# Kernel tuning notes

Measured on AMD Instinct MI355X. Metric: run time of the kernel, lower is better.

## Reference

```python
import jax, jax.numpy as jnp
from jax import lax
import numpy as np

B, C, H, W = 4, 256, 100, 100
K = 9  # num_points; deform kernel is [1, K], padding [0, K//2]


def conv2d(x, w, b, pad):
    # x: [B,Cin,H,W], w: [Cout,Cin,kh,kw]
    y = lax.conv_general_dilated(x, w, (1, 1), [(pad, pad), (pad, pad)],
                                 dimension_numbers=('NCHW', 'OIHW', 'NCHW'))
    return y + b[None, :, None, None]


def bilinear_sample(img, ys, xs):
    # img: [B,C,H,W]; ys, xs: [B,H,W] float sample coords; zero padding outside.
    Bs, Cs, Hs, Ws = img.shape
    y0f = jnp.floor(ys)
    x0f = jnp.floor(xs)
    wy = (ys - y0f)[:, None]  # [B,1,H,W]
    wx = (xs - x0f)[:, None]
    y0 = y0f.astype(jnp.int32)
    x0 = x0f.astype(jnp.int32)
    img_flat = img.reshape(Bs, Cs, Hs * Ws)

    def gather(yi, xi):
        valid = ((yi >= 0) & (yi < Hs) & (xi >= 0) & (xi < Ws))
        yc = jnp.clip(yi, 0, Hs - 1)
        xc = jnp.clip(xi, 0, Ws - 1)
        idx = (yc * Ws + xc).reshape(Bs, 1, Hs * Ws)
        v = jnp.take_along_axis(img_flat, idx, axis=2).reshape(Bs, Cs, Hs, Ws)
        return v * valid[:, None].astype(img.dtype)

    v00 = gather(y0, x0)
    v01 = gather(y0, x0 + 1)
    v10 = gather(y0 + 1, x0)
    v11 = gather(y0 + 1, x0 + 1)
    return (v00 * (1 - wy) * (1 - wx) + v01 * (1 - wy) * wx
            + v10 * wy * (1 - wx) + v11 * wy * wx)


def deform_conv_1xK(x, w, offset):
    # x: [B,C,H,W], w: [Cout,Cin,1,K], offset: [B,2K,H,W] with (dy,dx) per point.
    Bs, Cs, Hs, Ws = x.shape
    off = offset.reshape(Bs, K, 2, Hs, Ws)
    hh = jnp.arange(Hs, dtype=x.dtype)[:, None]
    ww = jnp.arange(Ws, dtype=x.dtype)[None, :]
    out = jnp.zeros((Bs, w.shape[0], Hs, Ws), dtype=x.dtype)
    for k in range(K):  # small fixed kernel loop
        ys = hh + off[:, k, 0]                    # kh=0, pad_h=0
        xs = ww + (k - K // 2) + off[:, k, 1]     # kw=k, pad_w=K//2
        s = bilinear_sample(x, ys, xs)            # [B,C,H,W]
        out = out + jnp.einsum('bchw,oc->bohw', s, w[:, :, 0, k])
    return out


def base_offset():
    dx = np.arange(-(K // 2), K // 2 + 1, dtype=np.float32)
    dy = np.zeros_like(dx)
    base = np.stack([dy, dx], axis=1).reshape(-1)  # [y0,x0,y1,x1,...]
    return jnp.asarray(base).reshape(1, 2 * K, 1, 1)


def setup_inputs() -> dict:
    key = jax.random.key(0)
    ks = jax.random.split(key, 8)
    return {
        'cls_feat': jax.random.normal(ks[0], (B, C, H, W), jnp.float32),
        'reg_feat': jax.random.normal(ks[1], (B, C, H, W), jnp.float32),
        'scale': jnp.float32(1.0),
        'offset_conv_w': 0.01 * jax.random.normal(ks[2], (C, C, 3, 3), jnp.float32),
        'offset_conv_b': jnp.zeros((C,), jnp.float32),
        'offset_out_w': 0.01 * jax.random.normal(ks[3], (2 * K, C, 1, 1), jnp.float32),
        'offset_out_b': jnp.zeros((2 * K,), jnp.float32),
        'cls_dcn_w': 0.02 * jax.random.normal(ks[4], (C, C, 1, K), jnp.float32),
        'reg_dcn_w': 0.02 * jax.random.normal(ks[5], (C, C, 1, K), jnp.float32),
    }


def reference(cls_feat, reg_feat, scale, offset_conv_w, offset_conv_b,
              offset_out_w, offset_out_b, cls_dcn_w, reg_dcn_w):
    # offset branch: ConvModule(3x3, ReLU) -> 1x1 conv -> learnable scalar
    t = jax.nn.relu(conv2d(reg_feat, offset_conv_w, offset_conv_b, 1))
    pts = scale * conv2d(t, offset_out_w, offset_out_b, 0)   # [B,2K,H,W]
    off = pts - base_offset()
    cls_out = jax.nn.relu(deform_conv_1xK(cls_feat, cls_dcn_w, off))
    reg_out = jax.nn.relu(deform_conv_1xK(reg_feat, reg_dcn_w, off))
    return (cls_out, reg_out, pts)
```

## Files before the change

### kernel.cpp

```cpp
#include <hip/hip_runtime.h>
#include <cstddef>

#define Bn 4
#define Cn 256
#define Hn 100
#define Wn 100
#define HWn 10000
#define Kn 9

typedef __attribute__((ext_vector_type(8))) short short8v;
typedef __attribute__((ext_vector_type(4))) float floatx4;
typedef __attribute__((ext_vector_type(4))) unsigned short ushort4v;

__device__ __forceinline__ float b2f(short s) {
  return __uint_as_float(((unsigned)(unsigned short)s) << 16);
}
__device__ __forceinline__ unsigned short f2bf(float f) {
  unsigned u = __float_as_uint(f);
  unsigned r = (u + 0x7FFF + ((u >> 16) & 1)) >> 16;
  return (unsigned short)r;
}
__device__ __forceinline__ void gload_lds16(const ushort* g, ushort* l) {
  __builtin_amdgcn_global_load_lds(
      (const __attribute__((address_space(1))) unsigned int*)(g),
      (__attribute__((address_space(3))) unsigned int*)(l), 16, 0, 0);
}

__global__ __launch_bounds__(256) void wtAll_kernel(
    const float* __restrict__ wcls, const float* __restrict__ wreg,
    const float* __restrict__ wconv, ushort* __restrict__ wtAll)
{
  int bk = blockIdx.x;
  int cc = bk & 7;
  int kk = (bk >> 3) % 9;
  int br = bk / 72;
  const float* w = (br == 0) ? wcls : (br == 1) ? wreg : wconv;
  ushort* dst = wtAll + (size_t)bk * 8192;
  for (int idx = threadIdx.x; idx < 8192; idx += 256) {
    int ot = idx >> 9;
    int l  = (idx >> 3) & 63;
    int j  = idx & 7;
    int o  = ot * 16 + (l & 15);
    int c  = cc * 32 + ((l >> 4) << 3) + j;
    dst[idx] = f2bf(w[((size_t)o * Cn + c) * Kn + kk]);
  }
}

__global__ __launch_bounds__(256) void ftrans_kernel(
    const float* __restrict__ clsf, const float* __restrict__ regf,
    ushort* __restrict__ ft)
{
  const int p0 = blockIdx.x * 32;
  const int c0 = blockIdx.y * 32;
  const int z  = blockIdx.z;
  const int br = z >> 2, b = z & 3;
  const float* src = (br ? regf : clsf) + (size_t)b * Cn * HWn;
  __shared__ float tl[32][33];
  const int tid = threadIdx.x;
  for (int i = tid; i < 1024; i += 256) {
    int c = i >> 5, p = i & 31;
    int pp = p0 + p;
    tl[p][c] = (pp < HWn) ? src[(size_t)(c0 + c) * HWn + pp] : 0.f;
  }
  __syncthreads();
  int p = tid >> 3;
  int c = (tid & 7) * 4;
  int pp = p0 + p;
  if (pp < HWn) {
    ushort4v v;
    v.x = f2bf(tl[p][c + 0]);
    v.y = f2bf(tl[p][c + 1]);
    v.z = f2bf(tl[p][c + 2]);
    v.w = f2bf(tl[p][c + 3]);
    *(ushort4v*)(ft + ((size_t)z * HWn + pp) * Cn + c0 + c) = v;
  }
}

__global__ __launch_bounds__(256) void conv3x3_offset_kernel(
    const ushort* __restrict__ ft, const ushort* __restrict__ wtC,
    const float* __restrict__ ocb, const float* __restrict__ oow,
    const float* __restrict__ oob, const float* __restrict__ scale_p,
    float* __restrict__ pts)
{
  const int p0  = blockIdx.x * 64;
  const int b   = blockIdx.z;
  const int tid = threadIdx.x;
  const int wv  = tid >> 6;
  const int lane = tid & 63;

  __shared__ ushort al[8192];
  __shared__ ushort sl[2048];
  __shared__ ushort tl[Cn * 64];

  floatx4 acc[4][4]{};

  const ushort* ftb = ft + (size_t)(4 + b) * HWn * Cn;

  const int px = p0 + lane;
  const bool pvalid = px < HWn;
  const int pxc = pvalid ? px : 0;
  const int y  = pxc / Wn;
  const int x  = pxc - y * Wn;
  const int sidx = (((lane >> 4) * 64) + (lane & 15) + (wv << 4)) * 8;

  for (int tap = 0; tap < 9; ++tap) {
    const int dy = tap / 3 - 1, dx = tap % 3 - 1;
    const int yy = y + dy, xx = x + dx;
    const bool valid = pvalid && (unsigned)yy < (unsigned)Hn
                              && (unsigned)xx < (unsigned)Wn;
    const int pofs = valid ? (yy * Wn + xx) * Cn : 0;

    for (int cc = 0; cc < 8; ++cc) {
      __syncthreads();
      {
        const ushort* src = wtC + (((size_t)tap * 8 + cc) << 13) + tid * 8;
#pragma unroll
        for (int i = 0; i < 4; ++i)
          gload_lds16(src + i * 2048, al + tid * 8 + i * 2048);
      }
      {
        short8v v{};
        if (valid) v = *(const short8v*)(ftb + pofs + cc * 32 + (wv << 3));
        *(short8v*)(sl + sidx) = v;
      }
      __syncthreads();
      short8v fb[4];
#pragma unroll
      for (int nt = 0; nt < 4; ++nt)
        fb[nt] = *(const short8v*)(sl + (nt * 64 + lane) * 8);
#pragma unroll
      for (int mt = 0; mt < 4; ++mt) {
        short8v fa = *(const short8v*)(al + (((wv * 4 + mt) * 64) + lane) * 8);
#pragma unroll
        for (int nt = 0; nt < 4; ++nt)
          acc[mt][nt] = __builtin_amdgcn_mfma_f32_16x16x32_bf16(
              fa, fb[nt], acc[mt][nt], 0, 0, 0);
      }
    }
  }

#pragma unroll
  for (int mt = 0; mt < 4; ++mt) {
    int o = wv * 64 + mt * 16 + ((lane >> 4) << 2);
#pragma unroll
    for (int nt = 0; nt < 4; ++nt) {
      int pcol = nt * 16 + (lane & 15);
      floatx4 a4 = acc[mt][nt];
#pragma unroll
      for (int r = 0; r < 4; ++r) {
        float v = a4[r] + ocb[o + r];
        v = v > 0.f ? v : 0.f;
        tl[(o + r) * 64 + pcol] = f2bf(v);
      }
    }
  }
  __syncthreads();

  const int jw = __builtin_amdgcn_readfirstlane(tid >> 6);
  const int pp = tid & 63;
  const float s = *scale_p;
  if (p0 + pp < HWn) {
    for (int j = jw; j < 18; j += 4) {
      float a = oob[j];
      const float* wrow = oow + (size_t)j * Cn;
      for (int c = 0; c < Cn; ++c)
        a += wrow[c] * b2f(tl[c * 64 + pp]);
      pts[((size_t)b * 18 + j) * HWn + p0 + pp] = s * a;
    }
  }
}

__global__ __launch_bounds__(256) void deform_mfma_kernel(
    const ushort* __restrict__ ft, const ushort* __restrict__ wtA,
    const float* __restrict__ pts, float* __restrict__ out)
{
  const int p0  = blockIdx.x * 64;
  const int z   = blockIdx.z;
  const int br  = z >> 2, b = z & 3;
  const int tid = threadIdx.x;
  const int wv  = tid >> 6;
  const int lane = tid & 63;

  __shared__ ushort al[8192];
  __shared__ ushort sl[2048];

  floatx4 acc[4][4]{};

  const ushort* ftb = ft + (size_t)z * HWn * Cn;
  const float*  pb  = pts + (size_t)b * 18 * HWn;
  const ushort* wA  = wtA + (size_t)br * 9 * 8 * 8192;

  const int px = p0 + lane;
  const bool pvalid = px < HWn;
  const int pxc = pvalid ? px : 0;
  const int hy  = pxc / Wn;
  const int wx0 = pxc - hy * Wn;
  const int sidx = (((lane >> 4) * 64) + (lane & 15) + (wv << 4)) * 8;

  for (int k = 0; k < Kn; ++k) {
    float w00 = 0, w01 = 0, w10 = 0, w11 = 0;
    int i00 = 0, i01 = 0, i10 = 0, i11 = 0;
    {
      float py  = pb[(size_t)(2 * k) * HWn + pxc];
      float pxo = pb[(size_t)(2 * k + 1) * HWn + pxc];
      float offx = pxo - (float)(k - 4);
      float ys   = (float)hy + py;
      float xsf  = (float)(wx0 + (k - 4)) + offx;
      float y0f = floorf(ys), x0f = floorf(xsf);
      float wy = ys - y0f, wx = xsf - x0f;
      int y0 = (int)y0f, x0 = (int)x0f;
      int y1 = y0 + 1, x1 = x0 + 1;
      bool vy0 = (unsigned)y0 < (unsigned)Hn, vy1 = (unsigned)y1 < (unsigned)Hn;
      bool vx0 = (unsigned)x0 < (unsigned)Wn, vx1 = (unsigned)x1 < (unsigned)Wn;
      int yc0 = min(max(y0, 0), Hn - 1), yc1 = min(max(y1, 0), Hn - 1);
      int xc0 = min(max(x0, 0), Wn - 1), xc1 = min(max(x1, 0), Wn - 1);
      i00 = (yc0 * Wn + xc0) * Cn; i01 = (yc0 * Wn + xc1) * Cn;
      i10 = (yc1 * Wn + xc0) * Cn; i11 = (yc1 * Wn + xc1) * Cn;
      float oy = 1.f - wy, ox = 1.f - wx;
      bool pv = pvalid;
      w00 = (pv && vy0 && vx0) ? oy * ox : 0.f;
      w01 = (pv && vy0 && vx1) ? oy * wx : 0.f;
      w10 = (pv && vy1 && vx0) ? wy * ox : 0.f;
      w11 = (pv && vy1 && vx1) ? wy * wx : 0.f;
    }

    for (int cc = 0; cc < 8; ++cc) {
      __syncthreads();
      {
        const ushort* src = wA + (((size_t)k * 8 + cc) << 13) + tid * 8;
#pragma unroll
        for (int i = 0; i < 4; ++i)
          gload_lds16(src + i * 2048, al + tid * 8 + i * 2048);
      }
      {
        const ushort* fbase = ftb + cc * 32 + (wv << 3);
        short8v c00 = *(const short8v*)(fbase + i00);
        short8v c01 = *(const short8v*)(fbase + i01);
        short8v c10 = *(const short8v*)(fbase + i10);
        short8v c11 = *(const short8v*)(fbase + i11);
        short8v r;
#pragma unroll
        for (int jj = 0; jj < 8; ++jj) {
          float v = w00 * b2f(c00[jj]) + w01 * b2f(c01[jj])
                  + w10 * b2f(c10[jj]) + w11 * b2f(c11[jj]);
          r[jj] = (short)f2bf(v);
        }
        *(short8v*)(sl + sidx) = r;
      }
      __syncthreads();
      short8v fb[4];
#pragma unroll
      for (int nt = 0; nt < 4; ++nt)
        fb[nt] = *(const short8v*)(sl + (nt * 64 + lane) * 8);
#pragma unroll
      for (int mt = 0; mt < 4; ++mt) {
        short8v fa = *(const short8v*)(al + (((wv * 4 + mt) * 64) + lane) * 8);
#pragma unroll
        for (int nt = 0; nt < 4; ++nt)
          acc[mt][nt] = __builtin_amdgcn_mfma_f32_16x16x32_bf16(
              fa, fb[nt], acc[mt][nt], 0, 0, 0);
      }
    }
  }

  float* ob = out + (size_t)br * Bn * Cn * HWn + (size_t)b * Cn * HWn;
#pragma unroll
  for (int mt = 0; mt < 4; ++mt) {
    int o = wv * 64 + mt * 16 + ((lane >> 4) << 2);
#pragma unroll
    for (int nt = 0; nt < 4; ++nt) {
      int p = p0 + nt * 16 + (lane & 15);
      if (p < HWn) {
        floatx4 a4 = acc[mt][nt];
#pragma unroll
        for (int r = 0; r < 4; ++r) {
          float v = a4[r];
          ob[(size_t)(o + r) * HWn + p] = v > 0.f ? v : 0.f;
        }
      }
    }
  }
}

extern "C" void kernel_launch(void* const* d_in, const int* in_sizes, int n_in,
                              void* d_out, int out_size, void* d_ws, size_t ws_size,
                              hipStream_t stream) {
  const float* cls_feat = (const float*)d_in[0];
  const float* reg_feat = (const float*)d_in[1];
  const float* scale    = (const float*)d_in[2];
  const float* ocw      = (const float*)d_in[3];
  const float* ocb      = (const float*)d_in[4];
  const float* oow      = (const float*)d_in[5];
  const float* oob      = (const float*)d_in[6];
  const float* wcls     = (const float*)d_in[7];
  const float* wreg     = (const float*)d_in[8];

  float* out_all = (float*)d_out;
  float* pts     = out_all + (size_t)2 * Bn * Cn * HWn;

  ushort* ft    = (ushort*)d_ws;
  ushort* wtAll = (ushort*)((char*)d_ws + (size_t)8 * HWn * Cn * 2);
  ushort* wtC   = wtAll + (size_t)2 * 9 * 8 * 8192;

  wtAll_kernel<<<dim3(216), 256, 0, stream>>>(wcls, wreg, ocw, wtAll);
  ftrans_kernel<<<dim3(313, 8, 8), 256, 0, stream>>>(cls_feat, reg_feat, ft);
  conv3x3_offset_kernel<<<dim3(157, 1, 4), 256, 0, stream>>>(
      ft, wtC, ocb, oow, oob, scale, pts);
  deform_mfma_kernel<<<dim3(157, 1, 8), 256, 0, stream>>>(
      ft, wtAll, pts, out_all);
}
```

Before: 591.5 us.

## Double-buffer LDS in conv and deform kernels and use MFMA for offset 1x1

Both the 3x3 offset conv and the deformable conv kernels now double-buffer weight and sampled-feature tiles in LDS. Global loads and bilinear gathers for the next chunk are issued before the current chunk's MFMAs, which removes one barrier per iteration and hides load latency. The 1x1 offset projection, previously a scalar loop over 256 channels per output, now runs as a bf16 MFMA with weights pre-packed by an extra block in the weight-prep kernel. This raises LDS use and register pressure, and rounds the 1x1 weights to bf16.

Result: faster. 512.9 us (-13.3%).

```diff
diff --git a/kernel.cpp b/kernel.cpp
--- a/kernel.cpp
+++ b/kernel.cpp
@@ -28,9 +28,22 @@
 
 __global__ __launch_bounds__(256) void wtAll_kernel(
     const float* __restrict__ wcls, const float* __restrict__ wreg,
-    const float* __restrict__ wconv, ushort* __restrict__ wtAll)
+    const float* __restrict__ wconv, const float* __restrict__ oow,
+    ushort* __restrict__ wtAll, ushort* __restrict__ oowA)
 {
   int bk = blockIdx.x;
+  if (bk == 216) {
+    for (int idx = threadIdx.x; idx < 8192; idx += 256) {
+      int j = idx & 7;
+      int l = (idx >> 3) & 63;
+      int q = idx >> 9;
+      int cc = q >> 1, ot = q & 1;
+      int o = ot * 16 + (l & 15);
+      int c = cc * 32 + ((l >> 4) << 3) + j;
+      oowA[idx] = (o < 18) ? f2bf(oow[(size_t)o * Cn + c]) : 0;
+    }
+    return;
+  }
   int cc = bk & 7;
   int kk = (bk >> 3) % 9;
   int br = bk / 72;
@@ -78,7 +91,7 @@
 
 __global__ __launch_bounds__(256) void conv3x3_offset_kernel(
     const ushort* __restrict__ ft, const ushort* __restrict__ wtC,
-    const float* __restrict__ ocb, const float* __restrict__ oow,
+    const float* __restrict__ ocb, const ushort* __restrict__ oowA,
     const float* __restrict__ oob, const float* __restrict__ scale_p,
     float* __restrict__ pts)
 {
@@ -88,9 +101,9 @@
   const int wv  = tid >> 6;
   const int lane = tid & 63;
 
-  __shared__ ushort al[8192];
-  __shared__ ushort sl[2048];
-  __shared__ ushort tl[Cn * 64];
+  __shared__ ushort smem[20480];
+  ushort* al = smem;
+  ushort* sl = smem + 16384;
 
   floatx4 acc[4][4]{};
 
@@ -103,71 +116,95 @@
   const int x  = pxc - y * Wn;
   const int sidx = (((lane >> 4) * 64) + (lane & 15) + (wv << 4)) * 8;
 
-  for (int tap = 0; tap < 9; ++tap) {
-    const int dy = tap / 3 - 1, dx = tap % 3 - 1;
-    const int yy = y + dy, xx = x + dx;
-    const bool valid = pvalid && (unsigned)yy < (unsigned)Hn
-                              && (unsigned)xx < (unsigned)Wn;
-    const int pofs = valid ? (yy * Wn + xx) * Cn : 0;
-
-    for (int cc = 0; cc < 8; ++cc) {
-      __syncthreads();
-      {
-        const ushort* src = wtC + (((size_t)tap * 8 + cc) << 13) + tid * 8;
-#pragma unroll
-        for (int i = 0; i < 4; ++i)
-          gload_lds16(src + i * 2048, al + tid * 8 + i * 2048);
+  int pofs = 0; bool valid = false;
+  auto tapgeo = [&](int tap) {
+    int dy = tap / 3 - 1, dx = tap % 3 - 1;
+    int yy = y + dy, xx = x + dx;
+    valid = pvalid && (unsigned)yy < (unsigned)Hn && (unsigned)xx < (unsigned)Wn;
+    pofs = valid ? (yy * Wn + xx) * Cn : 0;
+  };
+
+  short8v cv{};
+  tapgeo(0);
+  if (valid) cv = *(const short8v*)(ftb + pofs + (wv << 3));
+  {
+    const ushort* srcw = wtC + tid * 8;
+#pragma unroll
+    for (int i = 0; i < 4; ++i)
+      gload_lds16(srcw + i * 2048, al + tid * 8 + i * 2048);
+  }
+  *(short8v*)(sl + sidx) = cv;
+
+  for (int t = 0; t < 72; ++t) {
+    __syncthreads();
+    const int buf = t & 1, nb = buf ^ 1;
+    if (t < 71) {
+      const int t1 = t + 1, cc1 = t1 & 7;
+      if (cc1 == 0) tapgeo(t1 >> 3);
+      cv = short8v{};
+      if (valid) cv = *(const short8v*)(ftb + pofs + cc1 * 32 + (wv << 3));
+      const ushort* srcw = wtC + ((size_t)t1 << 13) + tid * 8;
+#pragma unroll
+      for (int i = 0; i < 4; ++i)
+        gload_lds16(srcw + i * 2048, al + nb * 8192 + tid * 8 + i * 2048);
+    }
+    short8v fbv[4];
+#pragma unroll
+    for (int nt = 0; nt < 4; ++nt)
+      fbv[nt] = *(const short8v*)(sl + buf * 2048 + (nt * 64 + lane) * 8);
+#pragma unroll
+    for (int mt = 0; mt < 4; ++mt) {
+      short8v fa = *(const short8v*)(al + buf * 8192 + (((wv * 4 + mt) * 64) + lane) * 8);
+#pragma unroll
+      for (int nt = 0; nt < 4; ++nt)
+        acc[mt][nt] = __builtin_amdgcn_mfma_f32_16x16x32_bf16(
+            fa, fbv[nt], acc[mt][nt], 0, 0, 0);
+    }
+    if (t < 71) *(short8v*)(sl + nb * 2048 + sidx) = cv;
+  }
+
+  __syncthreads();
+  ushort* tl = smem;
+#pragma unroll
+  for (int mt = 0; mt < 4; ++mt) {
+    int ob = wv * 64 + mt * 16 + ((lane >> 4) << 2);
+    floatx4 bv = *(const floatx4*)(ocb + ob);
+#pragma unroll
+    for (int nt = 0; nt < 4; ++nt) {
+      int pxl = nt * 16 + (lane & 15);
+      floatx4 a4 = acc[mt][nt];
+#pragma unroll
+      for (int rp = 0; rp < 4; rp += 2) {
+        float v0 = a4[rp]     + bv[rp];     v0 = v0 > 0.f ? v0 : 0.f;
+        float v1 = a4[rp + 1] + bv[rp + 1]; v1 = v1 > 0.f ? v1 : 0.f;
+        unsigned pk = (unsigned)f2bf(v0) | ((unsigned)f2bf(v1) << 16);
+        *(unsigned*)(tl + pxl * 264 + ob + rp) = pk;
       }
-      {
-        short8v v{};
-        if (valid) v = *(const short8v*)(ftb + pofs + cc * 32 + (wv << 3));
-        *(short8v*)(sl + sidx) = v;
-      }
-      __syncthreads();
-      short8v fb[4];
-#pragma unroll
-      for (int nt = 0; nt < 4; ++nt)
-        fb[nt] = *(const short8v*)(sl + (nt * 64 + lane) * 8);
-#pragma unroll
-      for (int mt = 0; mt < 4; ++mt) {
-        short8v fa = *(const short8v*)(al + (((wv * 4 + mt) * 64) + lane) * 8);
-#pragma unroll
-        for (int nt = 0; nt < 4; ++nt)
-          acc[mt][nt] = __builtin_amdgcn_mfma_f32_16x16x32_bf16(
-              fa, fb[nt], acc[mt][nt], 0, 0, 0);
-      }
-    }
-  }
-
-#pragma unroll
-  for (int mt = 0; mt < 4; ++mt) {
-    int o = wv * 64 + mt * 16 + ((lane >> 4) << 2);
-#pragma unroll
-    for (int nt = 0; nt < 4; ++nt) {
-      int pcol = nt * 16 + (lane & 15);
-      floatx4 a4 = acc[mt][nt];
-#pragma unroll
-      for (int r = 0; r < 4; ++r) {
-        float v = a4[r] + ocb[o + r];
-        v = v > 0.f ? v : 0.f;
-        tl[(o + r) * 64 + pcol] = f2bf(v);
-      }
     }
   }
   __syncthreads();
 
-  const int jw = __builtin_amdgcn_readfirstlane(tid >> 6);
-  const int pp = tid & 63;
+  floatx4 ap[2]{};
+#pragma unroll
+  for (int cc = 0; cc < 8; ++cc) {
+    short8v fbp = *(const short8v*)(tl + (wv * 16 + (lane & 15)) * 264
+                                    + cc * 32 + ((lane >> 4) << 3));
+#pragma unroll
+    for (int ot = 0; ot < 2; ++ot) {
+      short8v faw = *(const short8v*)(oowA + (((cc * 2 + ot) * 64) + lane) * 8);
+      ap[ot] = __builtin_amdgcn_mfma_f32_16x16x32_bf16(faw, fbp, ap[ot], 0, 0, 0);
+    }
+  }
   const float s = *scale_p;
-  if (p0 + pp < HWn) {
-    for (int j = jw; j < 18; j += 4) {
-      float a = oob[j];
-      const float* wrow = oow + (size_t)j * Cn;
-      for (int c = 0; c < Cn; ++c)
-        a += wrow[c] * b2f(tl[c * 64 + pp]);
-      pts[((size_t)b * 18 + j) * HWn + p0 + pp] = s * a;
-    }
-  }
+  const int pp = p0 + wv * 16 + (lane & 15);
+#pragma unroll
+  for (int ot = 0; ot < 2; ++ot)
+#pragma unroll
+    for (int r = 0; r < 4; ++r) {
+      int j = ot * 16 + ((lane >> 4) << 2) + r;
+      if (j < 18 && pp < HWn)
+        pts[((size_t)b * 18 + j) * HWn + pp] = s * (ap[ot][r] + oob[j]);
+    }
 }
 
 __global__ __launch_bounds__(256) void deform_mfma_kernel(
@@ -181,8 +218,9 @@
   const int wv  = tid >> 6;
   const int lane = tid & 63;
 
-  __shared__ ushort al[8192];
-  __shared__ ushort sl[2048];
+  __shared__ ushort smem[20480];
+  ushort* al = smem;
+  ushort* sl = smem + 16384;
 
   floatx4 acc[4][4]{};
 
@@ -197,69 +235,100 @@
   const int wx0 = pxc - hy * Wn;
   const int sidx = (((lane >> 4) * 64) + (lane & 15) + (wv << 4)) * 8;
 
-  for (int k = 0; k < Kn; ++k) {
-    float w00 = 0, w01 = 0, w10 = 0, w11 = 0;
-    int i00 = 0, i01 = 0, i10 = 0, i11 = 0;
-    {
-      float py  = pb[(size_t)(2 * k) * HWn + pxc];
-      float pxo = pb[(size_t)(2 * k + 1) * HWn + pxc];
-      float offx = pxo - (float)(k - 4);
-      float ys   = (float)hy + py;
-      float xsf  = (float)(wx0 + (k - 4)) + offx;
-      float y0f = floorf(ys), x0f = floorf(xsf);
-      float wy = ys - y0f, wx = xsf - x0f;
-      int y0 = (int)y0f, x0 = (int)x0f;
-      int y1 = y0 + 1, x1 = x0 + 1;
-      bool vy0 = (unsigned)y0 < (unsigned)Hn, vy1 = (unsigned)y1 < (unsigned)Hn;
-      bool vx0 = (unsigned)x0 < (unsigned)Wn, vx1 = (unsigned)x1 < (unsigned)Wn;
-      int yc0 = min(max(y0, 0), Hn - 1), yc1 = min(max(y1, 0), Hn - 1);
-      int xc0 = min(max(x0, 0), Wn - 1), xc1 = min(max(x1, 0), Wn - 1);
-      i00 = (yc0 * Wn + xc0) * Cn; i01 = (yc0 * Wn + xc1) * Cn;
-      i10 = (yc1 * Wn + xc0) * Cn; i11 = (yc1 * Wn + xc1) * Cn;
-      float oy = 1.f - wy, ox = 1.f - wx;
-      bool pv = pvalid;
-      w00 = (pv && vy0 && vx0) ? oy * ox : 0.f;
-      w01 = (pv && vy0 && vx1) ? oy * wx : 0.f;
-      w10 = (pv && vy1 && vx0) ? wy * ox : 0.f;
-      w11 = (pv && vy1 && vx1) ? wy * wx : 0.f;
-    }
-
-    for (int cc = 0; cc < 8; ++cc) {
-      __syncthreads();
-      {
-        const ushort* src = wA + (((size_t)k * 8 + cc) << 13) + tid * 8;
-#pragma unroll
-        for (int i = 0; i < 4; ++i)
-          gload_lds16(src + i * 2048, al + tid * 8 + i * 2048);
+  float w00 = 0, w01 = 0, w10 = 0, w11 = 0;
+  int i00 = 0, i01 = 0, i10 = 0, i11 = 0;
+  auto bilinear = [&](int k, float py, float pxo) {
+    float offx = pxo - (float)(k - 4);
+    float ys   = (float)hy + py;
+    float xsf  = (float)(wx0 + (k - 4)) + offx;
+    float y0f = floorf(ys), x0f = floorf(xsf);
+    float wy = ys - y0f, wx = xsf - x0f;
+    int y0 = (int)y0f, x0 = (int)x0f;
+    int y1 = y0 + 1, x1 = x0 + 1;
+    bool vy0 = (unsigned)y0 < (unsigned)Hn, vy1 = (unsigned)y1 < (unsigned)Hn;
+    bool vx0 = (unsigned)x0 < (unsigned)Wn, vx1 = (unsigned)x1 < (unsigned)Wn;
+    int yc0 = min(max(y0, 0), Hn - 1), yc1 = min(max(y1, 0), Hn - 1);
+    int xc0 = min(max(x0, 0), Wn - 1), xc1 = min(max(x1, 0), Wn - 1);
+    i00 = (yc0 * Wn + xc0) * Cn; i01 = (yc0 * Wn + xc1) * Cn;
+    i10 = (yc1 * Wn + xc0) * Cn; i11 = (yc1 * Wn + xc1) * Cn;
+    float oy = 1.f - wy, ox = 1.f - wx;
+    w00 = (pvalid && vy0 && vx0) ? oy * ox : 0.f;
+    w01 = (pvalid && vy0 && vx1) ? oy * wx : 0.f;
+    w10 = (pvalid && vy1 && vx0) ? wy * ox : 0.f;
+    w11 = (pvalid && vy1 && vx1) ? wy * wx : 0.f;
+  };
+
+  float pyN = pb[pxc];
+  float pxN = pb[(size_t)HWn + pxc];
+
+  bilinear(0, pyN, pxN);
+  pyN = pb[(size_t)2 * HWn + pxc];
+  pxN = pb[(size_t)3 * HWn + pxc];
+  short8v c00, c01, c10, c11;
+  {
+    const ushort* fbase = ftb + (wv << 3);
+    c00 = *(const short8v*)(fbase + i00);
+    c01 = *(const short8v*)(fbase + i01);
+    c10 = *(const short8v*)(fbase + i10);
+    c11 = *(const short8v*)(fbase + i11);
+    const ushort* srcw = wA + tid * 8;
+#pragma unroll
+    for (int i = 0; i < 4; ++i)
+      gload_lds16(srcw + i * 2048, al + tid * 8 + i * 2048);
+    short8v r;
+#pragma unroll
+    for (int jj = 0; jj < 8; ++jj) {
+      float v = w00 * b2f(c00[jj]) + w01 * b2f(c01[jj])
+              + w10 * b2f(c10[jj]) + w11 * b2f(c11[jj]);
+      r[jj] = (short)f2bf(v);
+    }
+    *(short8v*)(sl + sidx) = r;
+  }
+
+  for (int t = 0; t < 72; ++t) {
+    __syncthreads();
+    const int buf = t & 1, nb = buf ^ 1;
+    const bool more = t < 71;
+    if (more) {
+      const int t1 = t + 1, k1 = t1 >> 3, cc1 = t1 & 7;
+      if (cc1 == 0) {
+        bilinear(k1, pyN, pxN);
+        if (k1 < 8) {
+          pyN = pb[(size_t)(2 * k1 + 2) * HWn + pxc];
+          pxN = pb[(size_t)(2 * k1 + 3) * HWn + pxc];
+        }
       }
-      {
-        const ushort* fbase = ftb + cc * 32 + (wv << 3);
-        short8v c00 = *(const short8v*)(fbase + i00);
-        short8v c01 = *(const short8v*)(fbase + i01);
-        short8v c10 = *(const short8v*)(fbase + i10);
-        short8v c11 = *(const short8v*)(fbase + i11);
-        short8v r;
-#pragma unroll
-        for (int jj = 0; jj < 8; ++jj) {
-          float v = w00 * b2f(c00[jj]) + w01 * b2f(c01[jj])
-                  + w10 * b2f(c10[jj]) + w11 * b2f(c11[jj]);
-          r[jj] = (short)f2bf(v);
-        }
-        *(short8v*)(sl + sidx) = r;
+      const ushort* fbase = ftb + cc1 * 32 + (wv << 3);
+      c00 = *(const short8v*)(fbase + i00);
+      c01 = *(const short8v*)(fbase + i01);
+      c10 = *(const short8v*)(fbase + i10);
+      c11 = *(const short8v*)(fbase + i11);
+      const ushort* srcw = wA + ((size_t)t1 << 13) + tid * 8;
+#pragma unroll
+      for (int i = 0; i < 4; ++i)
+        gload_lds16(srcw + i * 2048, al + nb * 8192 + tid * 8 + i * 2048);
+    }
+    short8v fbv[4];
+#pragma unroll
+    for (int nt = 0; nt < 4; ++nt)
+      fbv[nt] = *(const short8v*)(sl + buf * 2048 + (nt * 64 + lane) * 8);
+#pragma unroll
+    for (int mt = 0; mt < 4; ++mt) {
+      short8v fa = *(const short8v*)(al + buf * 8192 + (((wv * 4 + mt) * 64) + lane) * 8);
+#pragma unroll
+      for (int nt = 0; nt < 4; ++nt)
+        acc[mt][nt] = __builtin_amdgcn_mfma_f32_16x16x32_bf16(
+            fa, fbv[nt], acc[mt][nt], 0, 0, 0);
+    }
+    if (more) {
+      short8v r;
+#pragma unroll
+      for (int jj = 0; jj < 8; ++jj) {
+        float v = w00 * b2f(c00[jj]) + w01 * b2f(c01[jj])
+                + w10 * b2f(c10[jj]) + w11 * b2f(c11[jj]);
+        r[jj] = (short)f2bf(v);
       }
-      __syncthreads();
-      short8v fb[4];
-#pragma unroll
-      for (int nt = 0; nt < 4; ++nt)
-        fb[nt] = *(const short8v*)(sl + (nt * 64 + lane) * 8);
-#pragma unroll
-      for (int mt = 0; mt < 4; ++mt) {
-        short8v fa = *(const short8v*)(al + (((wv * 4 + mt) * 64) + lane) * 8);
-#pragma unroll
-        for (int nt = 0; nt < 4; ++nt)
-          acc[mt][nt] = __builtin_amdgcn_mfma_f32_16x16x32_bf16(
-              fa, fb[nt], acc[mt][nt], 0, 0, 0);
-      }
+      *(short8v*)(sl + nb * 2048 + sidx) = r;
     }
   }
 
@@ -301,11 +370,12 @@
   ushort* ft    = (ushort*)d_ws;
   ushort* wtAll = (ushort*)((char*)d_ws + (size_t)8 * HWn * Cn * 2);
   ushort* wtC   = wtAll + (size_t)2 * 9 * 8 * 8192;
-
-  wtAll_kernel<<<dim3(216), 256, 0, stream>>>(wcls, wreg, ocw, wtAll);
+  ushort* oowA  = wtAll + (size_t)3 * 9 * 8 * 8192;
+
+  wtAll_kernel<<<dim3(217), 256, 0, stream>>>(wcls, wreg, ocw, oow, wtAll, oowA);
   ftrans_kernel<<<dim3(313, 8, 8), 256, 0, stream>>>(cls_feat, reg_feat, ft);
   conv3x3_offset_kernel<<<dim3(157, 1, 4), 256, 0, stream>>>(
-      ft, wtC, ocb, oow, oob, scale, pts);
+      ft, wtC, ocb, oowA, oob, scale, pts);
   deform_mfma_kernel<<<dim3(157, 1, 8), 256, 0, stream>>>(
       ft, wtAll, pts, out_all);
 }
```
